# Kernel optimization log

Hardware: AMD Instinct MI355X
Metric: run time of the kernel (lower is better)

## Reference

```python
import jax, jax.numpy as jnp
import numpy as np

B, L, DIM, K, V = 512, 200, 256, 2048, 100000


def setup_inputs() -> dict:
    key = jax.random.key(0)
    k1, k2, k3, k4, k5 = jax.random.split(key, 5)
    return {
        "history_item_ids": jax.random.randint(k1, (B, L), 0, V, dtype=jnp.int32),
        "history_item_masks": jax.random.randint(k2, (B, L), 0, 3, dtype=jnp.int32),
        "embedding_table": jax.random.normal(k3, (V, DIM), dtype=jnp.float32) * 0.1,
        "code_book": jax.random.normal(k4, (K, DIM), dtype=jnp.float32) * 0.1,
        "W_enc": jax.random.normal(k5, (2 * DIM, DIM), dtype=jnp.float32) * 0.05,
        "b_enc": jnp.zeros((DIM,), dtype=jnp.float32),
    }


def reference(history_item_ids, history_item_masks, embedding_table, code_book, W_enc, b_enc):
    # mask: valid history positions (>= 1)
    mask = (history_item_masks >= 1).astype(jnp.float32)            # [B, L]
    emb = embedding_table[history_item_ids] * mask[:, :, None]      # [B, L, D]
    # masked mean over history (eps matches the tf 1e-9)
    hist_mean = emb.sum(axis=1) / (mask.sum(axis=1, keepdims=True) + 1e-9)  # [B, D]
    # VQ quantization: pairwise squared distances, argmin, codebook gather
    flat = emb.reshape(-1, emb.shape[-1])                           # [B*L, D]
    distances = (
        jnp.sum(flat * flat, axis=1, keepdims=True)
        + jnp.sum(code_book * code_book, axis=1)
        - 2.0 * flat @ code_book.T
    )                                                               # [B*L, K]
    idx = jnp.argmin(distances, axis=1)                             # [B*L]
    vq = code_book[idx].reshape(emb.shape)                          # [B, L, D] (== one_hot @ code_book)
    vq_mean = vq.sum(axis=1) / mask.sum(axis=-1)[:, None]           # [B, D] (no eps in tf vqvae)
    x = jnp.concatenate([vq_mean, hist_mean], axis=-1)              # [B, 2D]
    return x @ W_enc + b_enc                                        # encoder dense -> [B, D]
```

## Files before the change

kernel.cpp:

```cpp
#include <hip/hip_runtime.h>
#include <hip/hip_bf16.h>
#include <cstddef>
#include <cstdint>

#define B_  512
#define L_  200
#define D_  256
#define K_  2048
#define BL_ (B_ * L_)

typedef __bf16 bf16x8 __attribute__((ext_vector_type(8)));
typedef float  f32x16 __attribute__((ext_vector_type(16)));

#define GL_LDS(g, l) __builtin_amdgcn_global_load_lds(                          \
    (const __attribute__((address_space(1))) void*)(g),                         \
    (__attribute__((address_space(3))) void*)(l), 16, 0, 0)

__device__ inline ushort f2bf(float f) {
    union { float f; uint u; } a; a.f = f;
    uint r = a.u + 0x7FFFu + ((a.u >> 16) & 1u);
    return (ushort)(r >> 16);
}

__global__ __launch_bounds__(256) void prep_kernel(const float* __restrict__ cb,
                                                   float* __restrict__ cnorm,
                                                   float* __restrict__ cnormR,
                                                   ushort* __restrict__ cbbf) {
    int code = (blockIdx.x * 256 + threadIdx.x) >> 6;
    int lane = threadIdx.x & 63;
    float4 v = ((const float4*)(cb + (size_t)code * D_))[lane];
    float s = v.x * v.x + v.y * v.y + v.z * v.z + v.w * v.w;
    #pragma unroll
    for (int off = 32; off; off >>= 1) s += __shfl_down(s, off);
    union { ushort us[4]; uint2 u2; } pk;
    pk.us[0] = f2bf(v.x); pk.us[1] = f2bf(v.y); pk.us[2] = f2bf(v.z); pk.us[3] = f2bf(v.w);
    ((uint2*)(cbbf + (size_t)code * D_))[lane] = pk.u2;
    if (lane == 0) {
        cnorm[code] = s;
        int r = code & 31;
        int h = (r >> 2) & 1;
        int j = (r & 3) | ((r >> 3) << 2);
        cnormR[(code & ~31) | (h << 4) | j] = s + 16.0f;
    }
}

__global__ __launch_bounds__(256) void kstar_kernel(const float* __restrict__ cnorm,
                                                    int* __restrict__ kstar) {
    __shared__ unsigned long long red[4];
    const int t = threadIdx.x;
    unsigned long long best = ~0ull;
    #pragma unroll
    for (int i = 0; i < K_ / 256; ++i) {
        int k = i * 256 + t;
        unsigned long long key = (((unsigned long long)__float_as_uint(cnorm[k])) << 11) | (unsigned)k;
        best = best < key ? best : key;
    }
    #pragma unroll
    for (int off = 32; off; off >>= 1) {
        unsigned long long o = __shfl_down(best, off);
        best = best < o ? best : o;
    }
    if ((t & 63) == 0) red[t >> 6] = best;
    __syncthreads();
    if (t == 0) {
        unsigned long long b = red[0];
        for (int i = 1; i < 4; ++i) b = b < red[i] ? b : red[i];
        kstar[0] = (int)(b & 0x7FFull);
    }
}

struct CN4 { float4 a, b, c, d; };

#define STAGE(CIDX, BASE) {                                                     \
    int wub = __builtin_amdgcn_readfirstlane((t >> 6) * 256);                   \
    _Pragma("unroll")                                                           \
    for (int i_ = 0; i_ < 4; ++i_) {                                            \
      int slot = wub + i_ * 64 + (t & 63);                                      \
      int n_ = slot >> 5, up_ = slot & 31;                                      \
      int u_ = up_ ^ (n_ & 7);                                                  \
      GL_LDS(cbbf + (((size_t)(((CIDX) << 5) + n_)) << 8) + (u_ << 3),          \
             (char*)(BASE) + (size_t)(wub + i_ * 64) * 16);                     \
    } }

#define PROCSEL(BASE, NC, CN) {                                                 \
    f32x16 A0, A1;                                                              \
    A0[0]=(CN).a.x; A0[1]=(CN).a.y; A0[2]=(CN).a.z; A0[3]=(CN).a.w;             \
    A0[4]=(CN).b.x; A0[5]=(CN).b.y; A0[6]=(CN).b.z; A0[7]=(CN).b.w;             \
    A0[8]=(CN).c.x; A0[9]=(CN).c.y; A0[10]=(CN).c.z; A0[11]=(CN).c.w;           \
    A0[12]=(CN).d.x; A0[13]=(CN).d.y; A0[14]=(CN).d.z; A0[15]=(CN).d.w;         \
    A1 = A0;                                                                    \
    _Pragma("unroll")                                                           \
    for (int s_ = 0; s_ < 16; ++s_) {                                           \
      bf16x8 aF = *(const bf16x8*)((const char*)(BASE) +                        \
                    (((l31 << 5) + ((2 * s_ + h) ^ swz)) << 4));                \
      A0 = __builtin_amdgcn_mfma_f32_32x32x16_bf16(aF, bfrag[0][s_], A0, 0,0,0);\
      A1 = __builtin_amdgcn_mfma_f32_32x32x16_bf16(aF, bfrag[1][s_], A1, 0,0,0);\
    }                                                                           \
    uint sb_ = (uint)((NC) << 5);                                               \
    _Pragma("unroll")                                                           \
    for (int jp_ = 0; jp_ < 8; ++jp_) {                                         \
      int j0_ = 2 * jp_, j1_ = 2 * jp_ + 1;                                     \
      uint c0_ = sb_ + (uint)((j0_ & 3) + 8 * (j0_ >> 2));                      \
      uint c1_ = sb_ + (uint)((j1_ & 3) + 8 * (j1_ >> 2));                      \
      {                                                                         \
        uint ka = (__float_as_uint(A0[j0_]) & 0xFFFFF800u) | (c0_ + h4);        \
        uint kb = (__float_as_uint(A0[j1_]) & 0xFFFFF800u) | (c1_ + h4);        \
        uint lo = min(ka, kb), hi = max(ka, kb);                                \
        uint tt = max(b1a, lo);                                                 \
        b1a = min(b1a, lo);                                                     \
        b2a = min(min(b2a, tt), hi);                                            \
      }                                                                         \
      {                                                                         \
        uint ka = (__float_as_uint(A1[j0_]) & 0xFFFFF800u) | (c0_ + h4);        \
        uint kb = (__float_as_uint(A1[j1_]) & 0xFFFFF800u) | (c1_ + h4);        \
        uint lo = min(ka, kb), hi = max(ka, kb);                                \
        uint tt = max(b1b, lo);                                                 \
        b1b = min(b1b, lo);                                                     \
        b2b = min(min(b2b, tt), hi);                                            \
      }                                                                         \
    } }

#define LDCN_LDS(NC, CN) {                                                      \
    const float4* cp_ = (const float4*)(cnlds + ((NC) << 5) + (h << 4));        \
    (CN).a = cp_[0]; (CN).b = cp_[1]; (CN).c = cp_[2]; (CN).d = cp_[3]; }

__global__ __launch_bounds__(256, 2) void gemm_top2_kernel(
    const int* __restrict__ ids, const int* __restrict__ masks,
    const float* __restrict__ table, const ushort* __restrict__ cbbf,
    const float* __restrict__ cnormR, uint2* __restrict__ cand) {

  __shared__ ushort cbuf[4 * 32 * 256];
  __shared__ float  cnlds[2048];

  const int t    = threadIdx.x;
  const int lane = t & 63;
  const int l31  = lane & 31;
  const int h    = lane >> 5;
  const int w    = t >> 6;
  const int ptile = blockIdx.x;
  const int swz  = l31 & 7;
  const uint h4  = (uint)(h << 2);

  bf16x8 bfrag[2][16];
  #pragma unroll
  for (int pt = 0; pt < 2; ++pt) {
    int pos = ptile * 256 + w * 64 + pt * 32 + l31;
    int id  = ids[pos];
    float m = (masks[pos] >= 1) ? -2.0f : 0.0f;
    const float* er = table + (size_t)id * D_ + 8 * h;
    #pragma unroll
    for (int s = 0; s < 16; ++s) {
      float4 x = *(const float4*)(er + 16 * s);
      float4 y = *(const float4*)(er + 16 * s + 4);
      bf16x8 b;
      b[0] = (__bf16)(x.x * m); b[1] = (__bf16)(x.y * m);
      b[2] = (__bf16)(x.z * m); b[3] = (__bf16)(x.w * m);
      b[4] = (__bf16)(y.x * m); b[5] = (__bf16)(y.y * m);
      b[6] = (__bf16)(y.z * m); b[7] = (__bf16)(y.w * m);
      bfrag[pt][s] = b;
    }
  }

  uint b1a = 0xFFFFFFFFu, b2a = 0xFFFFFFFFu;
  uint b1b = 0xFFFFFFFFu, b2b = 0xFFFFFFFFu;

  asm volatile("s_waitcnt vmcnt(0)" ::: "memory");
  __builtin_amdgcn_sched_barrier(0);

  {
    int wub2 = __builtin_amdgcn_readfirstlane((t >> 6) * 128);
    #pragma unroll
    for (int i = 0; i < 2; ++i) {
      int slot = wub2 + i * 64 + (t & 63);
      GL_LDS(cnormR + (size_t)slot * 4, (char*)cnlds + (size_t)(wub2 + i * 64) * 16);
    }
  }
  STAGE(0, (char*)cbuf);
  STAGE(1, (char*)cbuf + 16384);
  STAGE(2, (char*)cbuf + 32768);

  #pragma unroll 1
  for (int nc = 0; nc < 62; ++nc) {
    asm volatile("s_waitcnt vmcnt(8)" ::: "memory");
    __builtin_amdgcn_s_barrier();
    __builtin_amdgcn_sched_barrier(0);
    if (nc <= 60) {
      char* sb = (char*)cbuf + (size_t)(((nc + 3) & 3) * 16384);
      STAGE(nc + 3, sb);
    }
    CN4 cn; LDCN_LDS(nc, cn);
    char* rb = (char*)cbuf + (size_t)((nc & 3) * 16384);
    PROCSEL(rb, nc, cn);
  }
  {
    asm volatile("s_waitcnt vmcnt(4)" ::: "memory");
    __builtin_amdgcn_s_barrier();
    __builtin_amdgcn_sched_barrier(0);
    CN4 cn; LDCN_LDS(62, cn);
    PROCSEL((char*)cbuf + (size_t)((62 & 3) * 16384), 62, cn);
  }
  {
    asm volatile("s_waitcnt vmcnt(0)" ::: "memory");
    __builtin_amdgcn_s_barrier();
    __builtin_amdgcn_sched_barrier(0);
    CN4 cn; LDCN_LDS(63, cn);
    PROCSEL((char*)cbuf + (size_t)((63 & 3) * 16384), 63, cn);
  }

  {
    uint ob1 = __shfl_xor(b1a, 32), ob2 = __shfl_xor(b2a, 32);
    uint m1 = min(b1a, ob1);
    uint m2 = min(min(max(b1a, ob1), b2a), ob2);
    if (h == 0) cand[(size_t)(ptile * 256 + w * 64 + 0 * 32 + l31)] = make_uint2(m1, m2);
  }
  {
    uint ob1 = __shfl_xor(b1b, 32), ob2 = __shfl_xor(b2b, 32);
    uint m1 = min(b1b, ob1);
    uint m2 = min(min(max(b1b, ob1), b2b), ob2);
    if (h == 0) cand[(size_t)(ptile * 256 + w * 64 + 1 * 32 + l31)] = make_uint2(m1, m2);
  }
}

#define GRP 5

__global__ __launch_bounds__(512, 2) void tail_kernel(
    const int* __restrict__ ids, const int* __restrict__ masks,
    const float* __restrict__ table, const float* __restrict__ cb,
    const float* __restrict__ cnorm, const uint2* __restrict__ cand2,
    const int* __restrict__ kstar,
    float* __restrict__ gacc, int* __restrict__ gcnt) {

    __shared__ float red_vq[8][D_];
    __shared__ float red_e[8][D_];
    __shared__ int   redc[8];

    const int b  = blockIdx.x;
    const int t  = threadIdx.x;
    const int wv = t >> 6, lane = t & 63;

    const int ks = kstar[0];
    float4 ckstar = ((const float4*)(cb + (size_t)ks * D_))[lane];

    float4 vqa = make_float4(0.f, 0.f, 0.f, 0.f);
    float4 ea  = make_float4(0.f, 0.f, 0.f, 0.f);
    int cnta = 0, mcnt = 0;

    #pragma unroll 1
    for (int g = 0; g < 25 / GRP; ++g) {
        const int l0 = wv * 25 + g * GRP;

        uint2 kk[GRP];
        int   id[GRP];
        int   mk[GRP];
        #pragma unroll
        for (int j = 0; j < GRP; ++j) {
            int u = b * L_ + l0 + j;
            kk[j] = cand2[u];
            id[j] = ids[u];
            mk[j] = masks[u];
        }

        int k1[GRP], k2[GRP];
        bool valid[GRP], needy[GRP];
        #pragma unroll
        for (int j = 0; j < GRP; ++j) {
            uint g1 = kk[j].x;
            uint g2 = kk[j].y;
            k1[j] = (int)(g1 & 0x7FFu);
            k2[j] = (int)(g2 & 0x7FFu);
            valid[j] = (mk[j] >= 1);
            needy[j] = valid[j] && (((g2 & 0xFFFFF800u) - (g1 & 0xFFFFF800u)) < (3u << 11));
        }

        float4 e[GRP], c1[GRP], c2[GRP];
        #pragma unroll
        for (int j = 0; j < GRP; ++j)
            if (valid[j]) e[j] = ((const float4*)(table + (size_t)id[j] * D_))[lane];
        #pragma unroll
        for (int j = 0; j < GRP; ++j)
            if (valid[j]) c1[j] = ((const float4*)(cb + (size_t)k1[j] * D_))[lane];
        #pragma unroll
        for (int j = 0; j < GRP; ++j)
            if (needy[j]) c2[j] = ((const float4*)(cb + (size_t)k2[j] * D_))[lane];

        #pragma unroll
        for (int j = 0; j < GRP; ++j) {
            if (!valid[j]) { mcnt++; continue; }
            float4 ch = c1[j];
            if (needy[j]) {
                float d1 = fmaf(e[j].x, c1[j].x, fmaf(e[j].y, c1[j].y,
                            fmaf(e[j].z, c1[j].z, e[j].w * c1[j].w)));
                float d2 = fmaf(e[j].x, c2[j].x, fmaf(e[j].y, c2[j].y,
                            fmaf(e[j].z, c2[j].z, e[j].w * c2[j].w)));
                #pragma unroll
                for (int off = 32; off; off >>= 1) {
                    d1 += __shfl_xor(d1, off);
                    d2 += __shfl_xor(d2, off);
                }
                float s1 = cnorm[k1[j]] - 2.0f * d1;
                float s2 = cnorm[k2[j]] - 2.0f * d2;
                bool sel = (s2 < s1) || (s2 == s1 && k2[j] < k1[j]);
                ch = sel ? c2[j] : c1[j];
            }
            vqa.x += ch.x; vqa.y += ch.y; vqa.z += ch.z; vqa.w += ch.w;
            ea.x += e[j].x; ea.y += e[j].y; ea.z += e[j].z; ea.w += e[j].w;
            cnta++;
        }
    }

    float fm = (float)mcnt;
    vqa.x = fmaf(fm, ckstar.x, vqa.x);
    vqa.y = fmaf(fm, ckstar.y, vqa.y);
    vqa.z = fmaf(fm, ckstar.z, vqa.z);
    vqa.w = fmaf(fm, ckstar.w, vqa.w);

    *(float4*)&red_vq[wv][lane * 4] = vqa;
    *(float4*)&red_e[wv][lane * 4]  = ea;
    if (lane == 0) redc[wv] = cnta;
    __syncthreads();

    if (t < D_) {
        float vs = 0.f;
        #pragma unroll
        for (int wv2 = 0; wv2 < 8; ++wv2) vs += red_vq[wv2][t];
        gacc[(size_t)b * (2 * D_) + t] = vs;
    } else {
        int d = t - D_;
        float es = 0.f;
        #pragma unroll
        for (int wv2 = 0; wv2 < 8; ++wv2) es += red_e[wv2][d];
        gacc[(size_t)b * (2 * D_) + D_ + d] = es;
    }
    if (t == 0) {
        int c = 0;
        #pragma unroll
        for (int wv2 = 0; wv2 < 8; ++wv2) c += redc[wv2];
        gcnt[b] = c;
    }
}

__global__ __launch_bounds__(256) void dense_kernel(
    const float* __restrict__ gacc, const int* __restrict__ gcnt,
    const float* __restrict__ W, const float* __restrict__ bvec,
    float* __restrict__ out) {

    __shared__ float x[2 * D_];
    const int b = blockIdx.x;
    const int t = threadIdx.x;

    float fc = (float)gcnt[b];
    x[t]      = gacc[(size_t)b * (2 * D_) + t] / fc;
    x[D_ + t] = gacc[(size_t)b * (2 * D_) + D_ + t] / (fc + 1e-9f);
    __syncthreads();

    float acc = bvec[t];
    #pragma unroll 8
    for (int i = 0; i < 2 * D_; ++i)
        acc = fmaf(x[i], W[i * D_ + t], acc);
    out[(size_t)b * D_ + t] = acc;
}

extern "C" void kernel_launch(void* const* d_in, const int* in_sizes, int n_in,
                              void* d_out, int out_size, void* d_ws, size_t ws_size,
                              hipStream_t stream) {
    const int*   ids   = (const int*)  d_in[0];
    const int*   masks = (const int*)  d_in[1];
    const float* table = (const float*)d_in[2];
    const float* cb    = (const float*)d_in[3];
    const float* W     = (const float*)d_in[4];
    const float* bvec  = (const float*)d_in[5];
    float* out = (float*)d_out;

    char* p = (char*)d_ws;
    float*  cnorm  = (float*)p;             p += 8192;
    float*  cnormR = (float*)p;             p += 8192;
    ushort* cbbf   = (ushort*)p;            p += 1048576;
    uint2*  cand   = (uint2*)p;             p += (size_t)BL_ * 16;
    float*  gacc   = (float*)p;             p += (size_t)B_ * 2 * D_ * 4;
    int*    gcnt   = (int*)p;               p += B_ * 4;
    int*    kstar  = (int*)p;               p += 64;

    prep_kernel<<<K_ * 64 / 256, 256, 0, stream>>>(cb, cnorm, cnormR, cbbf);
    kstar_kernel<<<1, 256, 0, stream>>>(cnorm, kstar);
    gemm_top2_kernel<<<BL_ / 256, 256, 0, stream>>>(ids, masks, table, cbbf, cnormR, cand);
    tail_kernel<<<B_, 512, 0, stream>>>(ids, masks, table, cb, cnorm,
                                        cand, kstar, gacc, gcnt);
    dense_kernel<<<B_, 256, 0, stream>>>(gacc, gcnt, W, bvec, out);
}
```

Baseline: 313.3 us.

## Fuse kstar reduction into prep via atomicMin and dense layer into tail kernel

The min-norm code index is now found in prep_kernel with a per-block reduction and a 64-bit atomicMin on a workspace word that a memset resets to all ones. This removes the single-block kstar kernel launch. The dense encoder is folded into the tail kernel: each block normalises its pooled vectors in LDS and splits the 512x256 matvec into two halves across its 512 threads. That drops the gacc/gcnt round trip through global memory and one more launch, but adds a memset, an atomic, and more LDS per tail block, which may cut occupancy.

```diff
diff --git a/kernel.cpp b/kernel.cpp
--- a/kernel.cpp
+++ b/kernel.cpp
@@ -25,9 +25,12 @@
 __global__ __launch_bounds__(256) void prep_kernel(const float* __restrict__ cb,
                                                    float* __restrict__ cnorm,
                                                    float* __restrict__ cnormR,
-                                                   ushort* __restrict__ cbbf) {
+                                                   ushort* __restrict__ cbbf,
+                                                   unsigned long long* __restrict__ kmin) {
+    __shared__ unsigned long long pk4[4];
     int code = (blockIdx.x * 256 + threadIdx.x) >> 6;
     int lane = threadIdx.x & 63;
+    int wv   = threadIdx.x >> 6;
     float4 v = ((const float4*)(cb + (size_t)code * D_))[lane];
     float s = v.x * v.x + v.y * v.y + v.z * v.z + v.w * v.w;
     #pragma unroll
@@ -41,31 +44,14 @@
         int h = (r >> 2) & 1;
         int j = (r & 3) | ((r >> 3) << 2);
         cnormR[(code & ~31) | (h << 4) | j] = s + 16.0f;
-    }
-}
-
-__global__ __launch_bounds__(256) void kstar_kernel(const float* __restrict__ cnorm,
-                                                    int* __restrict__ kstar) {
-    __shared__ unsigned long long red[4];
-    const int t = threadIdx.x;
-    unsigned long long best = ~0ull;
-    #pragma unroll
-    for (int i = 0; i < K_ / 256; ++i) {
-        int k = i * 256 + t;
-        unsigned long long key = (((unsigned long long)__float_as_uint(cnorm[k])) << 11) | (unsigned)k;
-        best = best < key ? best : key;
-    }
-    #pragma unroll
-    for (int off = 32; off; off >>= 1) {
-        unsigned long long o = __shfl_down(best, off);
-        best = best < o ? best : o;
-    }
-    if ((t & 63) == 0) red[t >> 6] = best;
+        pk4[wv] = (((unsigned long long)__float_as_uint(s)) << 11) | (unsigned)code;
+    }
     __syncthreads();
-    if (t == 0) {
-        unsigned long long b = red[0];
-        for (int i = 1; i < 4; ++i) b = b < red[i] ? b : red[i];
-        kstar[0] = (int)(b & 0x7FFull);
+    if (threadIdx.x == 0) {
+        unsigned long long m = pk4[0];
+        #pragma unroll
+        for (int i = 1; i < 4; ++i) m = m < pk4[i] ? m : pk4[i];
+        atomicMin(kmin, m);
     }
 }
 
@@ -223,22 +209,25 @@
 
 #define GRP 5
 
-__global__ __launch_bounds__(512, 2) void tail_kernel(
+__global__ __launch_bounds__(512, 2) void finish_kernel(
     const int* __restrict__ ids, const int* __restrict__ masks,
     const float* __restrict__ table, const float* __restrict__ cb,
     const float* __restrict__ cnorm, const uint2* __restrict__ cand2,
-    const int* __restrict__ kstar,
-    float* __restrict__ gacc, int* __restrict__ gcnt) {
+    const unsigned long long* __restrict__ kmin,
+    const float* __restrict__ W, const float* __restrict__ bvec,
+    float* __restrict__ out) {
 
     __shared__ float red_vq[8][D_];
     __shared__ float red_e[8][D_];
     __shared__ int   redc[8];
+    __shared__ float xbuf[2 * D_];
+    __shared__ float part[2 * D_];
 
     const int b  = blockIdx.x;
     const int t  = threadIdx.x;
     const int wv = t >> 6, lane = t & 63;
 
-    const int ks = kstar[0];
+    const int ks = (int)(kmin[0] & 0x7FFull);
     float4 ckstar = ((const float4*)(cb + (size_t)ks * D_))[lane];
 
     float4 vqa = make_float4(0.f, 0.f, 0.f, 0.f);
@@ -319,45 +308,39 @@
     if (lane == 0) redc[wv] = cnta;
     __syncthreads();
 
-    if (t < D_) {
-        float vs = 0.f;
-        #pragma unroll
-        for (int wv2 = 0; wv2 < 8; ++wv2) vs += red_vq[wv2][t];
-        gacc[(size_t)b * (2 * D_) + t] = vs;
-    } else {
-        int d = t - D_;
-        float es = 0.f;
-        #pragma unroll
-        for (int wv2 = 0; wv2 < 8; ++wv2) es += red_e[wv2][d];
-        gacc[(size_t)b * (2 * D_) + D_ + d] = es;
-    }
-    if (t == 0) {
+    {
         int c = 0;
         #pragma unroll
-        for (int wv2 = 0; wv2 < 8; ++wv2) c += redc[wv2];
-        gcnt[b] = c;
-    }
-}
-
-__global__ __launch_bounds__(256) void dense_kernel(
-    const float* __restrict__ gacc, const int* __restrict__ gcnt,
-    const float* __restrict__ W, const float* __restrict__ bvec,
-    float* __restrict__ out) {
-
-    __shared__ float x[2 * D_];
-    const int b = blockIdx.x;
-    const int t = threadIdx.x;
-
-    float fc = (float)gcnt[b];
-    x[t]      = gacc[(size_t)b * (2 * D_) + t] / fc;
-    x[D_ + t] = gacc[(size_t)b * (2 * D_) + D_ + t] / (fc + 1e-9f);
+        for (int i = 0; i < 8; ++i) c += redc[i];
+        float fc = (float)c;
+        if (t < D_) {
+            float vs = 0.f;
+            #pragma unroll
+            for (int i = 0; i < 8; ++i) vs += red_vq[i][t];
+            xbuf[t] = vs / fc;
+        } else {
+            int d = t - D_;
+            float es = 0.f;
+            #pragma unroll
+            for (int i = 0; i < 8; ++i) es += red_e[i][d];
+            xbuf[D_ + d] = es / (fc + 1e-9f);
+        }
+    }
     __syncthreads();
 
-    float acc = bvec[t];
-    #pragma unroll 8
-    for (int i = 0; i < 2 * D_; ++i)
-        acc = fmaf(x[i], W[i * D_ + t], acc);
-    out[(size_t)b * D_ + t] = acc;
+    {
+        const int d  = t & (D_ - 1);
+        const int hh = t >> 8;
+        float acc = 0.f;
+        const float* Wp = W + (size_t)(hh * D_) * D_ + d;
+        #pragma unroll 8
+        for (int i = 0; i < D_; ++i)
+            acc = fmaf(xbuf[hh * D_ + i], Wp[i * D_], acc);
+        part[t] = acc;
+    }
+    __syncthreads();
+    if (t < D_)
+        out[(size_t)b * D_ + t] = bvec[t] + part[t] + part[D_ + t];
 }
 
 extern "C" void kernel_launch(void* const* d_in, const int* in_sizes, int n_in,
@@ -376,14 +359,11 @@
     float*  cnormR = (float*)p;             p += 8192;
     ushort* cbbf   = (ushort*)p;            p += 1048576;
     uint2*  cand   = (uint2*)p;             p += (size_t)BL_ * 16;
-    float*  gacc   = (float*)p;             p += (size_t)B_ * 2 * D_ * 4;
-    int*    gcnt   = (int*)p;               p += B_ * 4;
-    int*    kstar  = (int*)p;               p += 64;
-
-    prep_kernel<<<K_ * 64 / 256, 256, 0, stream>>>(cb, cnorm, cnormR, cbbf);
-    kstar_kernel<<<1, 256, 0, stream>>>(cnorm, kstar);
+    unsigned long long* kmin = (unsigned long long*)p; p += 64;
+
+    hipMemsetAsync(kmin, 0xFF, 8, stream);
+    prep_kernel<<<K_ * 64 / 256, 256, 0, stream>>>(cb, cnorm, cnormR, cbbf, kmin);
     gemm_top2_kernel<<<BL_ / 256, 256, 0, stream>>>(ids, masks, table, cbbf, cnormR, cand);
-    tail_kernel<<<B_, 512, 0, stream>>>(ids, masks, table, cb, cnorm,
-                                        cand, kstar, gacc, gcnt);
-    dense_kernel<<<B_, 256, 0, stream>>>(gacc, gcnt, W, bvec, out);
-}
+    finish_kernel<<<B_, 512, 0, stream>>>(ids, masks, table, cb, cnorm,
+                                          cand, kmin, W, bvec, out);
+}
```

Result: faster. 299.2 us (-4.5%).
